# Kernel tuning notes

Measured on AMD Instinct MI355X. Metric: run time of the kernel, lower is better.

The kernel has to match this reference:

```python
import jax, jax.numpy as jnp
import numpy as np

N_HEAD, D_MODEL, D_VOCAB = 8, 512, 32000
B, P = 8, 512


def setup_inputs() -> dict:
    key = jax.random.key(0)
    k_x, k_w, k_b = jax.random.split(key, 3)
    input_tensor = jax.random.normal(k_x, (B, P, N_HEAD, D_MODEL), dtype=jnp.float32)
    # per-head Linear params, torch layout: weight [d_vocab, d_model], bias [d_vocab]
    bound = 1.0 / np.sqrt(D_MODEL)
    weights = jax.random.uniform(k_w, (N_HEAD, D_VOCAB, D_MODEL), minval=-bound, maxval=bound, dtype=jnp.float32)
    biases = jax.random.uniform(k_b, (N_HEAD, D_VOCAB), minval=-bound, maxval=bound, dtype=jnp.float32)
    return {"input_tensor": input_tensor, "weights": weights, "biases": biases}


def reference(input_tensor, weights, biases) -> jnp.ndarray:
    # sum_h (x[:,:,h,:] @ W_h^T + b_h)  -> single contraction over (h, d)
    # input_tensor: [B, P, H, D]; weights: [H, V, D]; biases: [H, V]
    out = jnp.einsum("bphd,hvd->bpv", input_tensor, weights)
    out = out + biases.sum(axis=0)  # [V] broadcast over [B, P, V]
    return out
```

## Files before the change

### kernel.cpp

```cpp
#include <hip/hip_runtime.h>
#include <hip/hip_bf16.h>
#include <stdint.h>

#define NHEAD 8
#define DMODEL 512
#define DVOCAB 32000
#define M_DIM 4096
#define K_DIM 4096
#define N_DIM 32000
#define NT    64

typedef short bf16x8 __attribute__((ext_vector_type(8)));
typedef float f32x4 __attribute__((ext_vector_type(4)));
typedef unsigned short ushort8 __attribute__((ext_vector_type(8)));

template <int V> struct IC { static constexpr int v = V; };

__device__ __forceinline__ unsigned short f2bf(float f) {
    unsigned int u = __builtin_bit_cast(unsigned int, f);
    u = (u + 0x7fffu + ((u >> 16) & 1u)) >> 16;
    return (unsigned short)u;
}

__device__ __forceinline__ void load16_to_lds(const void* g, void* l) {
    __builtin_amdgcn_global_load_lds(
        (const __attribute__((address_space(1))) unsigned int*)g,
        (__attribute__((address_space(3))) unsigned int*)l, 16, 0, 0);
}

__global__ void cvt_x(const float* __restrict__ in, unsigned short* __restrict__ out) {
    long t = (long)blockIdx.x * 256 + threadIdx.x;
    const float4* s = (const float4*)in + t * 2;
    float4 a = s[0], b = s[1];
    ushort8 o;
    o[0] = f2bf(a.x); o[1] = f2bf(a.y); o[2] = f2bf(a.z); o[3] = f2bf(a.w);
    o[4] = f2bf(b.x); o[5] = f2bf(b.y); o[6] = f2bf(b.z); o[7] = f2bf(b.w);
    *(ushort8*)(out + t * 8) = o;
}

__global__ void cvt_w(const float* __restrict__ in, unsigned short* __restrict__ out) {
    int t = blockIdx.x * 256 + threadIdx.x;
    int d8 = t & 63;
    int hv = t >> 6;
    int h = hv / DVOCAB;
    int v = hv - h * DVOCAB;
    const float4* s = (const float4*)(in + (long)hv * DMODEL + d8 * 8);
    float4 a = s[0], b = s[1];
    ushort8 o;
    o[0] = f2bf(a.x); o[1] = f2bf(a.y); o[2] = f2bf(a.z); o[3] = f2bf(a.w);
    o[4] = f2bf(b.x); o[5] = f2bf(b.y); o[6] = f2bf(b.z); o[7] = f2bf(b.w);
    *(ushort8*)(out + (long)v * K_DIM + h * DMODEL + d8 * 8) = o;
}

__global__ void bias_red(const float* __restrict__ b, float* __restrict__ out) {
    int v = blockIdx.x * 256 + threadIdx.x;
    if (v >= DVOCAB) return;
    float s = 0.f;
    #pragma unroll
    for (int h = 0; h < NHEAD; ++h) s += b[h * DVOCAB + v];
    out[v] = s;
}

#define BAR()    __builtin_amdgcn_s_barrier()
#define VMCNT8() asm volatile("s_waitcnt vmcnt(8)" ::: "memory")
#define VMCNT6() asm volatile("s_waitcnt vmcnt(6)" ::: "memory")
#define VMCNT0() asm volatile("s_waitcnt vmcnt(0)" ::: "memory")

__global__ __launch_bounds__(512, 2) void gemm256(
    const unsigned short* __restrict__ A,
    const unsigned short* __restrict__ B,
    const float* __restrict__ bias,
    float* __restrict__ C)
{
    __shared__ __attribute__((aligned(16))) unsigned short lds[2][2][2][8192];

    const int tid = threadIdx.x;
    const int bid = blockIdx.x;
    const int wg = (bid & 7) * 250 + (bid >> 3);
    const int mt = wg & 15;
    const int nt = wg >> 4;
    const long m0 = (long)mt * 256;
    const long n0 = (long)nt * 256;

    const int wid = tid >> 6, lane = tid & 63;
    const int wr = wid >> 2, wc = wid & 3;
    const int lr = lane & 15, lk = lane >> 4;
    const int swz = lr & 7;

    const unsigned short* pA[2];
    const unsigned short* pB[2];
    #pragma unroll
    for (int ks = 0; ks < 2; ++ks) {
        const int ch = ((ks << 2) | lk) ^ swz;
        pA[ks] = &lds[0][0][0][0] + (wr * 64 + lr) * 64 + ch * 8;
        pB[ks] = &lds[1][0][0][0] + (wc * 32 + lr) * 64 + ch * 8;
    }
    #define LDA(mi, ks, HALF, CURB) \
        (*(const bf16x8*)(pA[ks] + (mi) * 1024 + (HALF) * 16384 + (CURB) * 8192))
    #define LDB(nj, ks, HALF, CURB) \
        (*(const bf16x8*)(pB[ks] + (nj) * 1024 + (HALF) * 16384 + (CURB) * 8192))

    const char* Ab = (const char*)(A + m0 * K_DIM);
    const char* Bb = (const char*)(B + n0 * K_DIM);
    const int row0 = tid >> 3,         c0 = (tid & 7) ^ (row0 & 7);
    const int row1 = (512 + tid) >> 3, c1 = ((512 + tid) & 7) ^ (row1 & 7);
    unsigned int a00 = (unsigned)(row0 * K_DIM + c0 * 8) * 2u;
    unsigned int a01 = (unsigned)(row1 * K_DIM + c1 * 8) * 2u;
    unsigned int a10 = (unsigned)((128 + row0) * K_DIM + c0 * 8) * 2u;
    unsigned int a11 = (unsigned)((128 + row1) * K_DIM + c1 * 8) * 2u;
    unsigned int b00 = a00, b01 = a01, b10 = a10, b11 = a11;

    #define ST_A0(CURB) do { \
        load16_to_lds(Ab + a00, (char*)&lds[0][0][(CURB)][0] + tid * 16); \
        load16_to_lds(Ab + a01, (char*)&lds[0][0][(CURB)][0] + 8192 + tid * 16); \
        a00 += 128; a01 += 128; } while (0)
    #define ST_A1(CURB) do { \
        load16_to_lds(Ab + a10, (char*)&lds[0][1][(CURB)][0] + tid * 16); \
        load16_to_lds(Ab + a11, (char*)&lds[0][1][(CURB)][0] + 8192 + tid * 16); \
        a10 += 128; a11 += 128; } while (0)
    #define ST_B0(CURB) do { \
        load16_to_lds(Bb + b00, (char*)&lds[1][0][(CURB)][0] + tid * 16); \
        load16_to_lds(Bb + b01, (char*)&lds[1][0][(CURB)][0] + 8192 + tid * 16); \
        b00 += 128; b01 += 128; } while (0)
    #define ST_B1(CURB) do { \
        load16_to_lds(Bb + b10, (char*)&lds[1][1][(CURB)][0] + tid * 16); \
        load16_to_lds(Bb + b11, (char*)&lds[1][1][(CURB)][0] + 8192 + tid * 16); \
        b10 += 128; b11 += 128; } while (0)

    #define MFQUAD(AF, BF, MO, NO) do {                                        \
        _Pragma("unroll")                                                      \
        for (int ks = 0; ks < 2; ++ks)                                         \
            _Pragma("unroll")                                                  \
            for (int mi = 0; mi < 4; ++mi)                                     \
                _Pragma("unroll")                                              \
                for (int nj = 0; nj < 2; ++nj)                                 \
                    acc[(MO) + mi][(NO) + nj] =                                \
                        __builtin_amdgcn_mfma_f32_16x16x32_bf16(               \
                            AF[mi][ks], BF[nj][ks], acc[(MO) + mi][(NO) + nj], \
                            0, 0, 0);                                          \
    } while (0)

    f32x4 acc[8][4];
    #pragma unroll
    for (int i = 0; i < 8; ++i)
        #pragma unroll
        for (int j = 0; j < 4; ++j)
            acc[i][j] = (f32x4){0.f, 0.f, 0.f, 0.f};

    bf16x8 afL[4][2], afH[4][2], bf0[2][2], bf1[2][2];

    ST_A0(0); ST_B0(0); ST_B1(0); ST_A1(0);
    ST_A0(1); ST_B0(1); ST_B1(1); ST_A1(1);
    VMCNT8();
    BAR();
    #pragma unroll
    for (int mi = 0; mi < 4; ++mi) {
        afL[mi][0] = LDA(mi, 0, 0, 0);
        afL[mi][1] = LDA(mi, 1, 0, 0);
    }
    #pragma unroll
    for (int nj = 0; nj < 2; ++nj) {
        bf0[nj][0] = LDB(nj, 0, 0, 0);
        bf0[nj][1] = LDB(nj, 1, 0, 0);
    }

    auto body = [&](auto curc, int t) {
        constexpr int CUR = decltype(curc)::v;

        #pragma unroll
        for (int nj = 0; nj < 2; ++nj) {
            bf1[nj][0] = LDB(nj, 0, 1, CUR);
            bf1[nj][1] = LDB(nj, 1, 1, CUR);
        }
        __builtin_amdgcn_s_setprio(1);
        MFQUAD(afL, bf0, 0, 0);
        __builtin_amdgcn_s_setprio(0);
        BAR();

        if (t + 2 < NT) { ST_A0(CUR); ST_B0(CUR); }
        #pragma unroll
        for (int mi = 0; mi < 4; ++mi) {
            afH[mi][0] = LDA(mi, 0, 1, CUR);
            afH[mi][1] = LDA(mi, 1, 1, CUR);
        }
        __builtin_amdgcn_s_setprio(1);
        MFQUAD(afL, bf1, 0, 2);
        __builtin_amdgcn_s_setprio(0);
        BAR();

        if (t + 2 < NT) ST_B1(CUR);
        __builtin_amdgcn_s_setprio(1);
        MFQUAD(afH, bf0, 4, 0);
        __builtin_amdgcn_s_setprio(0);
        if (t < NT - 2) { VMCNT6(); } else { VMCNT0(); }
        BAR();

        if (t + 2 < NT) ST_A1(CUR);
        if (t + 1 < NT) {
            #pragma unroll
            for (int mi = 0; mi < 4; ++mi) {
                afL[mi][0] = LDA(mi, 0, 0, CUR ^ 1);
                afL[mi][1] = LDA(mi, 1, 0, CUR ^ 1);
            }
            #pragma unroll
            for (int nj = 0; nj < 2; ++nj) {
                bf0[nj][0] = LDB(nj, 0, 0, CUR ^ 1);
                bf0[nj][1] = LDB(nj, 1, 0, CUR ^ 1);
            }
        }
        __builtin_amdgcn_s_setprio(1);
        MFQUAD(afH, bf1, 4, 2);
        __builtin_amdgcn_s_setprio(0);
    };

    for (int t = 0; t < NT; t += 2) {
        body(IC<0>{}, t);
        body(IC<1>{}, t + 1);
    }
    #undef LDA
    #undef LDB
    #undef ST_A0
    #undef ST_A1
    #undef ST_B0
    #undef ST_B1
    #undef MFQUAD

    #pragma unroll
    for (int nj = 0; nj < 4; ++nj) {
        const long col = n0 + (nj >> 1) * 128 + wc * 32 + (nj & 1) * 16 + lr;
        const float bs = bias[col];
        #pragma unroll
        for (int mi = 0; mi < 8; ++mi) {
            const long row = m0 + (mi >> 2) * 128 + wr * 64 + (mi & 3) * 16 + lk * 4;
            #pragma unroll
            for (int r = 0; r < 4; ++r)
                __builtin_nontemporal_store(acc[mi][nj][r] + bs,
                                            &C[(row + r) * (long)N_DIM + col]);
        }
    }
}

__global__ void naive_out(const float* __restrict__ x, const float* __restrict__ w,
                          const float* __restrict__ b, float* __restrict__ out) {
    long idx = (long)blockIdx.x * 256 + threadIdx.x;
    if (idx >= (long)M_DIM * N_DIM) return;
    long m = idx / N_DIM;
    int v = (int)(idx - m * N_DIM);
    float s = 0.f;
    for (int h = 0; h < NHEAD; ++h) {
        const float* xr = x + m * K_DIM + h * DMODEL;
        const float* wr = w + ((long)h * DVOCAB + v) * DMODEL;
        float ps = 0.f;
        for (int d = 0; d < DMODEL; ++d) ps += xr[d] * wr[d];
        s += ps + b[h * DVOCAB + v];
    }
    out[idx] = s;
}

extern "C" void kernel_launch(void* const* d_in, const int* in_sizes, int n_in,
                              void* d_out, int out_size, void* d_ws, size_t ws_size,
                              hipStream_t stream) {
    const float* x = (const float*)d_in[0];
    const float* w = (const float*)d_in[1];
    const float* b = (const float*)d_in[2];
    float* out = (float*)d_out;

    const size_t xbf_bytes = (size_t)M_DIM * K_DIM * 2;
    const size_t wbf_bytes = (size_t)N_DIM * K_DIM * 2;
    const size_t bs_bytes  = (size_t)N_DIM * 4;
    const size_t need = xbf_bytes + wbf_bytes + bs_bytes;

    if (ws_size < need) {
        long total = (long)M_DIM * N_DIM;
        int blocks = (int)((total + 255) / 256);
        naive_out<<<blocks, 256, 0, stream>>>(x, w, b, out);
        return;
    }

    unsigned short* xbf = (unsigned short*)d_ws;
    unsigned short* wbf = (unsigned short*)((char*)d_ws + xbf_bytes);
    float* bsum = (float*)((char*)d_ws + xbf_bytes + wbf_bytes);

    cvt_x<<<8192, 256, 0, stream>>>(x, xbf);
    cvt_w<<<64000, 256, 0, stream>>>(w, wbf);
    bias_red<<<125, 256, 0, stream>>>(b, bsum);
    gemm256<<<2000, 512, 0, stream>>>(xbf, wbf, bsum, out);
}
```

Measured before the change: 1.183 ms.

## Restructure GEMM pipeline into 8-phase schedule with single A fragment and XCD-grouped tile mapping

Reworks the main loop into a more synchronized phase schedule. Each quarter-MFQUAD is now bracketed by barriers, and LDS reads plus global-to-LDS stores are interleaved before each compute phase. A single A fragment register set replaces the low/high pair, which lowers register pressure. The prologue drops the ST_A1(1) prefetch and now issues it inside the loop. Block-to-tile mapping changes so that each XCD handles two M-tiles across a range of N-tiles, to improve L2 reuse of B. The extra barriers may cost throughput in exchange for fewer registers and tighter ordering.

```diff
diff --git a/kernel.cpp b/kernel.cpp
--- a/kernel.cpp
+++ b/kernel.cpp
@@ -62,7 +62,6 @@
 }
 
 #define BAR()    __builtin_amdgcn_s_barrier()
-#define VMCNT8() asm volatile("s_waitcnt vmcnt(8)" ::: "memory")
 #define VMCNT6() asm volatile("s_waitcnt vmcnt(6)" ::: "memory")
 #define VMCNT0() asm volatile("s_waitcnt vmcnt(0)" ::: "memory")
 
@@ -76,9 +75,9 @@
 
     const int tid = threadIdx.x;
     const int bid = blockIdx.x;
-    const int wg = (bid & 7) * 250 + (bid >> 3);
-    const int mt = wg & 15;
-    const int nt = wg >> 4;
+    const int xcd = bid & 7, j = bid >> 3;
+    const int mt = xcd * 2 + (j & 1);
+    const int nt = j >> 1;
     const long m0 = (long)mt * 256;
     const long n0 = (long)nt * 256;
 
@@ -144,73 +143,67 @@
     #pragma unroll
     for (int i = 0; i < 8; ++i)
         #pragma unroll
-        for (int j = 0; j < 4; ++j)
-            acc[i][j] = (f32x4){0.f, 0.f, 0.f, 0.f};
-
-    bf16x8 afL[4][2], afH[4][2], bf0[2][2], bf1[2][2];
+        for (int jn = 0; jn < 4; ++jn)
+            acc[i][jn] = (f32x4){0.f, 0.f, 0.f, 0.f};
+
+    bf16x8 af[4][2], bf0[2][2], bf1[2][2];
 
     ST_A0(0); ST_B0(0); ST_B1(0); ST_A1(0);
-    ST_A0(1); ST_B0(1); ST_B1(1); ST_A1(1);
-    VMCNT8();
+    ST_A0(1); ST_B0(1); ST_B1(1);
+    VMCNT6();
     BAR();
-    #pragma unroll
-    for (int mi = 0; mi < 4; ++mi) {
-        afL[mi][0] = LDA(mi, 0, 0, 0);
-        afL[mi][1] = LDA(mi, 1, 0, 0);
-    }
-    #pragma unroll
-    for (int nj = 0; nj < 2; ++nj) {
-        bf0[nj][0] = LDB(nj, 0, 0, 0);
-        bf0[nj][1] = LDB(nj, 1, 0, 0);
-    }
 
     auto body = [&](auto curc, int t) {
         constexpr int CUR = decltype(curc)::v;
+
+        #pragma unroll
+        for (int mi = 0; mi < 4; ++mi) {
+            af[mi][0] = LDA(mi, 0, 0, CUR);
+            af[mi][1] = LDA(mi, 1, 0, CUR);
+        }
+        #pragma unroll
+        for (int nj = 0; nj < 2; ++nj) {
+            bf0[nj][0] = LDB(nj, 0, 0, CUR);
+            bf0[nj][1] = LDB(nj, 1, 0, CUR);
+        }
+        if (t + 1 < NT) ST_A1(CUR ^ 1);
+        BAR();
+        __builtin_amdgcn_s_setprio(1);
+        MFQUAD(af, bf0, 0, 0);
+        __builtin_amdgcn_s_setprio(0);
+        BAR();
 
         #pragma unroll
         for (int nj = 0; nj < 2; ++nj) {
             bf1[nj][0] = LDB(nj, 0, 1, CUR);
             bf1[nj][1] = LDB(nj, 1, 1, CUR);
         }
-        __builtin_amdgcn_s_setprio(1);
-        MFQUAD(afL, bf0, 0, 0);
-        __builtin_amdgcn_s_setprio(0);
-        BAR();
-
-        if (t + 2 < NT) { ST_A0(CUR); ST_B0(CUR); }
+        if (t + 2 < NT) ST_A0(CUR);
+        BAR();
+        __builtin_amdgcn_s_setprio(1);
+        MFQUAD(af, bf1, 0, 2);
+        __builtin_amdgcn_s_setprio(0);
+        BAR();
+
         #pragma unroll
         for (int mi = 0; mi < 4; ++mi) {
-            afH[mi][0] = LDA(mi, 0, 1, CUR);
-            afH[mi][1] = LDA(mi, 1, 1, CUR);
-        }
-        __builtin_amdgcn_s_setprio(1);
-        MFQUAD(afL, bf1, 0, 2);
+            af[mi][0] = LDA(mi, 0, 1, CUR);
+            af[mi][1] = LDA(mi, 1, 1, CUR);
+        }
+        if (t + 2 < NT) ST_B0(CUR);
+        BAR();
+        __builtin_amdgcn_s_setprio(1);
+        MFQUAD(af, bf0, 4, 0);
         __builtin_amdgcn_s_setprio(0);
         BAR();
 
         if (t + 2 < NT) ST_B1(CUR);
-        __builtin_amdgcn_s_setprio(1);
-        MFQUAD(afH, bf0, 4, 0);
-        __builtin_amdgcn_s_setprio(0);
         if (t < NT - 2) { VMCNT6(); } else { VMCNT0(); }
         BAR();
-
-        if (t + 2 < NT) ST_A1(CUR);
-        if (t + 1 < NT) {
-            #pragma unroll
-            for (int mi = 0; mi < 4; ++mi) {
-                afL[mi][0] = LDA(mi, 0, 0, CUR ^ 1);
-                afL[mi][1] = LDA(mi, 1, 0, CUR ^ 1);
-            }
-            #pragma unroll
-            for (int nj = 0; nj < 2; ++nj) {
-                bf0[nj][0] = LDB(nj, 0, 0, CUR ^ 1);
-                bf0[nj][1] = LDB(nj, 1, 0, CUR ^ 1);
-            }
-        }
-        __builtin_amdgcn_s_setprio(1);
-        MFQUAD(afH, bf1, 4, 2);
-        __builtin_amdgcn_s_setprio(0);
+        __builtin_amdgcn_s_setprio(1);
+        MFQUAD(af, bf1, 4, 2);
+        __builtin_amdgcn_s_setprio(0);
+        BAR();
     };
 
     for (int t = 0; t < NT; t += 2) {
```

Result: faster. 1.081 ms (median of 2 runs) (-8.6%).
